# Kernel optimization log

Measured on AMD Instinct MI355X. Metric: run time of the kernel, lower is better.

## Reference

```python
import jax, jax.numpy as jnp
import numpy as np

B, S, D_IN, D_OUT = 4, 2048, 4096, 4096
QMAX = 16  # 2**bits

def setup_inputs() -> dict:
    key = jax.random.key(0)
    k1, k2, k3, k4, k5 = jax.random.split(key, 5)
    x = jax.random.normal(k1, (B, S, D_IN), dtype=jnp.float32)
    weight_q = jax.random.randint(k2, (D_OUT, D_IN), 0, QMAX, dtype=jnp.int32)
    scale = jax.random.uniform(k3, (), dtype=jnp.float32) * 0.01 + 1e-4
    zero_point = jax.random.uniform(k4, (), dtype=jnp.float32) * QMAX
    bias = jax.random.normal(k5, (D_OUT,), dtype=jnp.float32)
    return {"x": x, "weight_q": weight_q, "scale": scale,
            "zero_point": zero_point, "bias": bias}

def reference(x, weight_q, scale, zero_point, bias):
    # Dequantize: w = (q - zero_point) * scale, then y = x @ w.T + b
    w = (weight_q.astype(jnp.float32) - zero_point) * scale  # [out, in]
    return jnp.einsum('bsi,oi->bso', x, w) + bias
```

## Files before the change

kernel.cpp:

```cpp
#include <hip/hip_runtime.h>
#include <cstdint>

#define M_DIM 8192
#define N_DIM 4096
#define K_DIM 4096

typedef int   i32x4 __attribute__((ext_vector_type(4)));
typedef float f32x4 __attribute__((ext_vector_type(4)));

__device__ __forceinline__ void gload_lds16(const void* g, void* l) {
  __builtin_amdgcn_global_load_lds(
      (const __attribute__((address_space(1))) unsigned int*)(uintptr_t)g,
      (__attribute__((address_space(3))) unsigned int*)(uintptr_t)l,
      16, 0, 0);
}

__global__ __launch_bounds__(256) void prep_kernel(
    const float* __restrict__ x, const int* __restrict__ q,
    signed char* __restrict__ xq, signed char* __restrict__ wq8,
    float* __restrict__ sx, float* __restrict__ si) {
  const int tid = threadIdx.x;
  if (blockIdx.x < M_DIM) {
    const int row = blockIdx.x;
    const float* xr = x + (size_t)row * K_DIM;
    signed char* xo = xq + (size_t)row * K_DIM;
    float4 v[4];
    float amax = 0.f;
#pragma unroll
    for (int j = 0; j < 4; ++j) {
      v[j] = *(const float4*)(xr + j * 1024 + tid * 4);
      amax = fmaxf(amax, fmaxf(fmaxf(fabsf(v[j].x), fabsf(v[j].y)),
                               fmaxf(fabsf(v[j].z), fabsf(v[j].w))));
    }
#pragma unroll
    for (int off = 32; off > 0; off >>= 1)
      amax = fmaxf(amax, __shfl_down(amax, off, 64));
    __shared__ float wred[4];
    __shared__ int   ired[4];
    if ((tid & 63) == 0) wred[tid >> 6] = amax;
    __syncthreads();
    amax = fmaxf(fmaxf(wred[0], wred[1]), fmaxf(wred[2], wred[3]));
    const float inv = amax > 0.f ? 127.f / amax : 0.f;
    int isum = 0;
#pragma unroll
    for (int j = 0; j < 4; ++j) {
      int ix = __float2int_rn(v[j].x * inv);
      int iy = __float2int_rn(v[j].y * inv);
      int iz = __float2int_rn(v[j].z * inv);
      int iw = __float2int_rn(v[j].w * inv);
      isum += ix + iy + iz + iw;
      char4 o; o.x = (char)ix; o.y = (char)iy; o.z = (char)iz; o.w = (char)iw;
      *(char4*)(xo + j * 1024 + tid * 4) = o;
    }
#pragma unroll
    for (int off = 32; off > 0; off >>= 1)
      isum += __shfl_down(isum, off, 64);
    if ((tid & 63) == 0) ired[tid >> 6] = isum;
    __syncthreads();
    if (tid == 0) {
      sx[row] = amax * (1.f / 127.f);
      si[row] = (float)(ired[0] + ired[1] + ired[2] + ired[3]);
    }
  } else {
    const int row = blockIdx.x - M_DIM;
    const int* qr = q + (size_t)row * K_DIM;
    signed char* wo = wq8 + (size_t)row * K_DIM;
#pragma unroll
    for (int j = 0; j < 4; ++j) {
      const int idx = j * 1024 + tid * 4;
      int4 v = *(const int4*)(qr + idx);
      char4 o; o.x = (char)v.x; o.y = (char)v.y; o.z = (char)v.z; o.w = (char)v.w;
      *(char4*)(wo + idx) = o;
    }
  }
}

__global__ __launch_bounds__(256) void qlinear_gemm_kernel(
    const signed char* __restrict__ A,
    const signed char* __restrict__ Bm,
    const float* __restrict__ sx,
    const float* __restrict__ si,
    const float* __restrict__ scale_p, const float* __restrict__ zp_p,
    const float* __restrict__ bias,
    float* __restrict__ out) {
  __shared__ signed char sA[128 * 64];
  __shared__ signed char sB[128 * 64];
  const int tid  = threadIdx.x;
  const int lane = tid & 63;
  const int wave = tid >> 6;
  const int bm = blockIdx.y * 128;
  const int bn = blockIdx.x * 128;
  const int wm = (wave & 1) * 64;
  const int wn = (wave >> 1) * 64;
  const int lr   = lane & 15;
  const int quad = lane >> 4;

  const int ld_row = lane >> 2;
  const int ld_col = ((lane & 3) ^ ((lane >> 3) & 3)) * 16;
  const signed char* ag = A  + (size_t)(bm + wave * 16 + ld_row) * K_DIM + ld_col;
  const signed char* bg = Bm + (size_t)(bn + wave * 16 + ld_row) * K_DIM + ld_col;
  signed char* sa_dst = sA + wave * 1024;
  signed char* sb_dst = sB + wave * 1024;

  const int swz = (quad ^ ((lr >> 1) & 3)) * 16;

  i32x4 acc[4][4] = {};

  for (int k0 = 0; k0 < K_DIM; k0 += 64) {
    gload_lds16(ag + k0,                       sa_dst);
    gload_lds16(ag + (size_t)64 * K_DIM + k0,  sa_dst + 4096);
    gload_lds16(bg + k0,                       sb_dst);
    gload_lds16(bg + (size_t)64 * K_DIM + k0,  sb_dst + 4096);
    __syncthreads();

    i32x4 av[4], bv[4];
#pragma unroll
    for (int i = 0; i < 4; ++i)
      av[i] = *(const i32x4*)(sA + (wm + i * 16 + lr) * 64 + swz);
#pragma unroll
    for (int j = 0; j < 4; ++j)
      bv[j] = *(const i32x4*)(sB + (wn + j * 16 + lr) * 64 + swz);
#pragma unroll
    for (int i = 0; i < 4; ++i)
#pragma unroll
      for (int j = 0; j < 4; ++j)
        acc[i][j] = __builtin_amdgcn_mfma_i32_16x16x64_i8(av[i], bv[j], acc[i][j], 0, 0, 0);
    __syncthreads();
  }

  const float scale = *scale_p;
  const float zp    = *zp_p;
#pragma unroll
  for (int i = 0; i < 4; ++i) {
    const int gm0 = bm + wm + i * 16 + quad * 4;
    float am[4], cm[4];
#pragma unroll
    for (int r = 0; r < 4; ++r) {
      am[r] = scale * sx[gm0 + r];
      cm[r] = -am[r] * zp * si[gm0 + r];
    }
#pragma unroll
    for (int j = 0; j < 4; ++j) {
      const int gn = bn + wn + j * 16 + lr;
      const float bb = bias[gn];
#pragma unroll
      for (int r = 0; r < 4; ++r)
        out[(size_t)(gm0 + r) * N_DIM + gn] =
            am[r] * (float)acc[i][j][r] + cm[r] + bb;
    }
  }
}

extern "C" void kernel_launch(void* const* d_in, const int* in_sizes, int n_in,
                              void* d_out, int out_size, void* d_ws, size_t ws_size,
                              hipStream_t stream) {
  const float* x     = (const float*)d_in[0];
  const int*   wq    = (const int*)d_in[1];
  const float* scale = (const float*)d_in[2];
  const float* zp    = (const float*)d_in[3];
  const float* bias  = (const float*)d_in[4];
  float* out = (float*)d_out;

  signed char* xq  = (signed char*)d_ws;
  signed char* wq8 = xq + (size_t)M_DIM * K_DIM;
  float* sx = (float*)(wq8 + (size_t)N_DIM * K_DIM);
  float* si = sx + M_DIM;

  prep_kernel<<<M_DIM + N_DIM, 256, 0, stream>>>(x, wq, xq, wq8, sx, si);
  dim3 grid(N_DIM / 128, M_DIM / 128);
  qlinear_gemm_kernel<<<grid, 256, 0, stream>>>(xq, wq8, sx, si, scale, zp, bias, out);
}
```

Before: 428.3 us.

## Rewrite int8 GEMM as 256x256 double-buffered pipelined tile and restructure prep

The GEMM moves from a 128x128 tile with 4 waves and a single LDS buffer to a 256x256 tile with 8 waves and K=128 per step. It double-buffers LDS, issues next-tile global->LDS loads in quarters between MFMA phases under manual vmcnt waits, and uses s_setprio around MFMA bursts. The prep kernel now quantizes one row per wave, using xor shuffles in place of LDS reductions, and converts weights with a grid-stride loop over fewer blocks. The aim is more data reuse per loaded byte and hiding global load latency behind MFMA work. The cost is much higher register and LDS pressure (128KB of LDS), and the hand-counted waits are fragile.

Measured after the change: 385.7 us. 10.0% less time.

```diff
diff --git a/kernel.cpp b/kernel.cpp
--- a/kernel.cpp
+++ b/kernel.cpp
@@ -4,9 +4,9 @@
 #define M_DIM 8192
 #define N_DIM 4096
 #define K_DIM 4096
-
-typedef int   i32x4 __attribute__((ext_vector_type(4)));
-typedef float f32x4 __attribute__((ext_vector_type(4)));
+#define NT    32
+
+typedef int i32x4 __attribute__((ext_vector_type(4)));
 
 __device__ __forceinline__ void gload_lds16(const void* g, void* l) {
   __builtin_amdgcn_global_load_lds(
@@ -19,63 +19,60 @@
     const float* __restrict__ x, const int* __restrict__ q,
     signed char* __restrict__ xq, signed char* __restrict__ wq8,
     float* __restrict__ sx, float* __restrict__ si) {
-  const int tid = threadIdx.x;
-  if (blockIdx.x < M_DIM) {
-    const int row = blockIdx.x;
+  const int tid  = threadIdx.x;
+  const int lane = tid & 63;
+  const int wv   = tid >> 6;
+  if (blockIdx.x < 2048) {
+    const int row = blockIdx.x * 4 + wv;
     const float* xr = x + (size_t)row * K_DIM;
     signed char* xo = xq + (size_t)row * K_DIM;
-    float4 v[4];
+    float4 v[16];
     float amax = 0.f;
 #pragma unroll
-    for (int j = 0; j < 4; ++j) {
-      v[j] = *(const float4*)(xr + j * 1024 + tid * 4);
+    for (int j = 0; j < 16; ++j) {
+      v[j] = *(const float4*)(xr + j * 256 + lane * 4);
       amax = fmaxf(amax, fmaxf(fmaxf(fabsf(v[j].x), fabsf(v[j].y)),
                                fmaxf(fabsf(v[j].z), fabsf(v[j].w))));
     }
 #pragma unroll
     for (int off = 32; off > 0; off >>= 1)
-      amax = fmaxf(amax, __shfl_down(amax, off, 64));
-    __shared__ float wred[4];
-    __shared__ int   ired[4];
-    if ((tid & 63) == 0) wred[tid >> 6] = amax;
-    __syncthreads();
-    amax = fmaxf(fmaxf(wred[0], wred[1]), fmaxf(wred[2], wred[3]));
+      amax = fmaxf(amax, __shfl_xor(amax, off, 64));
     const float inv = amax > 0.f ? 127.f / amax : 0.f;
     int isum = 0;
 #pragma unroll
-    for (int j = 0; j < 4; ++j) {
+    for (int j = 0; j < 16; ++j) {
       int ix = __float2int_rn(v[j].x * inv);
       int iy = __float2int_rn(v[j].y * inv);
       int iz = __float2int_rn(v[j].z * inv);
       int iw = __float2int_rn(v[j].w * inv);
       isum += ix + iy + iz + iw;
       char4 o; o.x = (char)ix; o.y = (char)iy; o.z = (char)iz; o.w = (char)iw;
-      *(char4*)(xo + j * 1024 + tid * 4) = o;
+      *(char4*)(xo + j * 256 + lane * 4) = o;
     }
 #pragma unroll
     for (int off = 32; off > 0; off >>= 1)
-      isum += __shfl_down(isum, off, 64);
-    if ((tid & 63) == 0) ired[tid >> 6] = isum;
-    __syncthreads();
-    if (tid == 0) {
+      isum += __shfl_xor(isum, off, 64);
+    if (lane == 0) {
       sx[row] = amax * (1.f / 127.f);
-      si[row] = (float)(ired[0] + ired[1] + ired[2] + ired[3]);
+      si[row] = (float)isum;
     }
   } else {
-    const int row = blockIdx.x - M_DIM;
-    const int* qr = q + (size_t)row * K_DIM;
-    signed char* wo = wq8 + (size_t)row * K_DIM;
-#pragma unroll
-    for (int j = 0; j < 4; ++j) {
-      const int idx = j * 1024 + tid * 4;
-      int4 v = *(const int4*)(qr + idx);
-      char4 o; o.x = (char)v.x; o.y = (char)v.y; o.z = (char)v.z; o.w = (char)v.w;
-      *(char4*)(wo + idx) = o;
-    }
-  }
-}
-
-__global__ __launch_bounds__(256) void qlinear_gemm_kernel(
+    const int bid = blockIdx.x - 2048;
+    const size_t total  = (size_t)N_DIM * K_DIM;
+    const size_t stride = (size_t)1024 * 4096;
+    for (size_t base = (size_t)bid * 4096; base < total; base += stride) {
+#pragma unroll
+      for (int u = 0; u < 4; ++u) {
+        const size_t idx = base + (size_t)u * 1024 + tid * 4;
+        int4 w = *(const int4*)(q + idx);
+        char4 o; o.x = (char)w.x; o.y = (char)w.y; o.z = (char)w.z; o.w = (char)w.w;
+        *(char4*)(wq8 + idx) = o;
+      }
+    }
+  }
+}
+
+__global__ __launch_bounds__(512) void qlinear_gemm_kernel(
     const signed char* __restrict__ A,
     const signed char* __restrict__ Bm,
     const float* __restrict__ sx,
@@ -83,56 +80,143 @@
     const float* __restrict__ scale_p, const float* __restrict__ zp_p,
     const float* __restrict__ bias,
     float* __restrict__ out) {
-  __shared__ signed char sA[128 * 64];
-  __shared__ signed char sB[128 * 64];
+  __shared__ signed char sA[2][2][16384];
+  __shared__ signed char sB[2][2][16384];
+
   const int tid  = threadIdx.x;
   const int lane = tid & 63;
-  const int wave = tid >> 6;
-  const int bm = blockIdx.y * 128;
-  const int bn = blockIdx.x * 128;
-  const int wm = (wave & 1) * 64;
-  const int wn = (wave >> 1) * 64;
+  const int w    = tid >> 6;
+  const int wr   = w >> 2;
+  const int wc   = w & 3;
   const int lr   = lane & 15;
   const int quad = lane >> 4;
 
-  const int ld_row = lane >> 2;
-  const int ld_col = ((lane & 3) ^ ((lane >> 3) & 3)) * 16;
-  const signed char* ag = A  + (size_t)(bm + wave * 16 + ld_row) * K_DIM + ld_col;
-  const signed char* bg = Bm + (size_t)(bn + wave * 16 + ld_row) * K_DIM + ld_col;
-  signed char* sa_dst = sA + wave * 1024;
-  signed char* sb_dst = sB + wave * 1024;
-
-  const int swz = (quad ^ ((lr >> 1) & 3)) * 16;
-
-  i32x4 acc[4][4] = {};
-
-  for (int k0 = 0; k0 < K_DIM; k0 += 64) {
-    gload_lds16(ag + k0,                       sa_dst);
-    gload_lds16(ag + (size_t)64 * K_DIM + k0,  sa_dst + 4096);
-    gload_lds16(bg + k0,                       sb_dst);
-    gload_lds16(bg + (size_t)64 * K_DIM + k0,  sb_dst + 4096);
-    __syncthreads();
-
-    i32x4 av[4], bv[4];
-#pragma unroll
-    for (int i = 0; i < 4; ++i)
-      av[i] = *(const i32x4*)(sA + (wm + i * 16 + lr) * 64 + swz);
-#pragma unroll
-    for (int j = 0; j < 4; ++j)
-      bv[j] = *(const i32x4*)(sB + (wn + j * 16 + lr) * 64 + swz);
-#pragma unroll
-    for (int i = 0; i < 4; ++i)
-#pragma unroll
-      for (int j = 0; j < 4; ++j)
-        acc[i][j] = __builtin_amdgcn_mfma_i32_16x16x64_i8(av[i], bv[j], acc[i][j], 0, 0, 0);
-    __syncthreads();
-  }
+  const int bm = blockIdx.y * 256;
+  const int bn = blockIdx.x * 256;
+
+  const int srow = lane >> 3;
+  const int cg   = (lane & 7) ^ srow;
+  const signed char* aG = A  + (size_t)(bm + w * 8 + srow) * K_DIM + cg * 16;
+  const signed char* bG = Bm + (size_t)(bn + w * 8 + srow) * K_DIM + cg * 16;
+  const int dwoff = w * 1024;
+
+#define STG_A(dst, h, c, t) \
+  gload_lds16(aG + (size_t)((h) * 128 + (c) * 64) * K_DIM + (size_t)(t) * 128, \
+              (dst) + (h) * 16384 + (c) * 8192 + dwoff)
+#define STG_B(dst, h, c, t) \
+  gload_lds16(bG + (size_t)((h) * 128 + (c) * 64) * K_DIM + (size_t)(t) * 128, \
+              (dst) + (h) * 16384 + (c) * 8192 + dwoff)
+
+  int off[2];
+#pragma unroll
+  for (int ks = 0; ks < 2; ++ks)
+    off[ks] = lr * 128 + (((ks * 4 + quad) ^ (lr & 7)) * 16);
+
+  i32x4 acc[8][4] = {};
+  i32x4 afr[4][2];
+  i32x4 bfr[2][2][2];
+
+  {
+    signed char* dA = &sA[0][0][0];
+    signed char* dB = &sB[0][0][0];
+    STG_B(dB, 0, 0, 0); STG_B(dB, 0, 1, 0);
+    STG_B(dB, 1, 0, 0); STG_B(dB, 1, 1, 0);
+    STG_A(dA, 0, 0, 0); STG_A(dA, 1, 0, 0);
+    STG_A(dA, 0, 1, 0); STG_A(dA, 1, 1, 0);
+  }
+
+  for (int t = 0; t < NT; ++t) {
+    const int buf = t & 1;
+    const signed char* pA = &sA[buf][wr][0];
+    const signed char* pB = &sB[buf][wc >> 1][0] + (wc & 1) * 8192;
+    signed char* nA = &sA[buf ^ 1][0][0];
+    signed char* nB = &sB[buf ^ 1][0][0];
+    const bool st = (t + 1) < NT;
+    const int tn = t + 1;
+
+    asm volatile("s_waitcnt vmcnt(2)" ::: "memory");
+    if (st) { STG_B(nB, 0, 0, tn); STG_B(nB, 0, 1, tn); }
+    __builtin_amdgcn_s_barrier();
+#pragma unroll
+    for (int m = 0; m < 4; ++m)
+#pragma unroll
+      for (int ks = 0; ks < 2; ++ks)
+        afr[m][ks] = *(const i32x4*)(pA + m * 2048 + off[ks]);
+#pragma unroll
+    for (int n = 0; n < 2; ++n)
+#pragma unroll
+      for (int ks = 0; ks < 2; ++ks)
+        bfr[0][n][ks] = *(const i32x4*)(pB + n * 2048 + off[ks]);
+    __builtin_amdgcn_s_setprio(1);
+#pragma unroll
+    for (int m = 0; m < 4; ++m)
+#pragma unroll
+      for (int n = 0; n < 2; ++n)
+#pragma unroll
+        for (int ks = 0; ks < 2; ++ks)
+          acc[m][n] = __builtin_amdgcn_mfma_i32_16x16x64_i8(
+              afr[m][ks], bfr[0][n][ks], acc[m][n], 0, 0, 0);
+    __builtin_amdgcn_s_setprio(0);
+
+    if (st) { STG_B(nB, 1, 0, tn); STG_B(nB, 1, 1, tn); }
+    __builtin_amdgcn_s_barrier();
+#pragma unroll
+    for (int n = 0; n < 2; ++n)
+#pragma unroll
+      for (int ks = 0; ks < 2; ++ks)
+        bfr[1][n][ks] = *(const i32x4*)(pB + 4096 + n * 2048 + off[ks]);
+    __builtin_amdgcn_s_setprio(1);
+#pragma unroll
+    for (int m = 0; m < 4; ++m)
+#pragma unroll
+      for (int n = 0; n < 2; ++n)
+#pragma unroll
+        for (int ks = 0; ks < 2; ++ks)
+          acc[m][2 + n] = __builtin_amdgcn_mfma_i32_16x16x64_i8(
+              afr[m][ks], bfr[1][n][ks], acc[m][2 + n], 0, 0, 0);
+    __builtin_amdgcn_s_setprio(0);
+
+    if (st) asm volatile("s_waitcnt vmcnt(4)" ::: "memory");
+    else    asm volatile("s_waitcnt vmcnt(0)" ::: "memory");
+    if (st) { STG_A(nA, 0, 0, tn); STG_A(nA, 1, 0, tn); }
+    __builtin_amdgcn_s_barrier();
+#pragma unroll
+    for (int m = 0; m < 4; ++m)
+#pragma unroll
+      for (int ks = 0; ks < 2; ++ks)
+        afr[m][ks] = *(const i32x4*)(pA + 8192 + m * 2048 + off[ks]);
+    __builtin_amdgcn_s_setprio(1);
+#pragma unroll
+    for (int m = 0; m < 4; ++m)
+#pragma unroll
+      for (int n = 0; n < 2; ++n)
+#pragma unroll
+        for (int ks = 0; ks < 2; ++ks)
+          acc[4 + m][n] = __builtin_amdgcn_mfma_i32_16x16x64_i8(
+              afr[m][ks], bfr[0][n][ks], acc[4 + m][n], 0, 0, 0);
+    __builtin_amdgcn_s_setprio(0);
+
+    if (st) { STG_A(nA, 0, 1, tn); STG_A(nA, 1, 1, tn); }
+    __builtin_amdgcn_s_barrier();
+    __builtin_amdgcn_s_setprio(1);
+#pragma unroll
+    for (int m = 0; m < 4; ++m)
+#pragma unroll
+      for (int n = 0; n < 2; ++n)
+#pragma unroll
+        for (int ks = 0; ks < 2; ++ks)
+          acc[4 + m][2 + n] = __builtin_amdgcn_mfma_i32_16x16x64_i8(
+              afr[m][ks], bfr[1][n][ks], acc[4 + m][2 + n], 0, 0, 0);
+    __builtin_amdgcn_s_setprio(0);
+  }
+#undef STG_A
+#undef STG_B
 
   const float scale = *scale_p;
   const float zp    = *zp_p;
 #pragma unroll
-  for (int i = 0; i < 4; ++i) {
-    const int gm0 = bm + wm + i * 16 + quad * 4;
+  for (int i = 0; i < 8; ++i) {
+    const int gm0 = bm + wr * 128 + i * 16 + quad * 4;
     float am[4], cm[4];
 #pragma unroll
     for (int r = 0; r < 4; ++r) {
@@ -141,7 +225,7 @@
     }
 #pragma unroll
     for (int j = 0; j < 4; ++j) {
-      const int gn = bn + wn + j * 16 + lr;
+      const int gn = bn + wc * 64 + j * 16 + lr;
       const float bb = bias[gn];
 #pragma unroll
       for (int r = 0; r < 4; ++r)
@@ -166,7 +250,7 @@
   float* sx = (float*)(wq8 + (size_t)N_DIM * K_DIM);
   float* si = sx + M_DIM;
 
-  prep_kernel<<<M_DIM + N_DIM, 256, 0, stream>>>(x, wq, xq, wq8, sx, si);
-  dim3 grid(N_DIM / 128, M_DIM / 128);
-  qlinear_gemm_kernel<<<grid, 256, 0, stream>>>(xq, wq8, sx, si, scale, zp, bias, out);
-}
+  prep_kernel<<<3072, 256, 0, stream>>>(x, wq, xq, wq8, sx, si);
+  dim3 grid(N_DIM / 256, M_DIM / 256);
+  qlinear_gemm_kernel<<<grid, 512, 0, stream>>>(xq, wq8, sx, si, scale, zp, bias, out);
+}
```
